# Kernel optimization log

Hardware: AMD Instinct MI355X
Metric: run time of the kernel (lower is better)

## Reference

```python
import jax, jax.numpy as jnp
import numpy as np

IOU_TH = 0.5      # iou_threshold
SCORE_TH = 0.5    # confidence_threshold (passed as score_threshold to tf NMS)
MAX_DET = 512     # max_detections


def setup_inputs() -> dict:
    key = jax.random.key(0)
    k1, k2, k3 = jax.random.split(key, 3)
    B, N, C = 8, 2048, 80
    # tf.image.non_max_suppression interprets box columns as corners
    # (y1, x1, y2, x2); generate valid corner boxes in [0, 1].
    mins = jax.random.uniform(k1, (B, N, 2), dtype=jnp.float32)
    sizes = jax.random.uniform(k2, (B, N, 2), dtype=jnp.float32) * 0.2 + 0.01
    box_prediction = jnp.concatenate([mins, mins + sizes], axis=-1)  # [B,N,4]
    class_prediction = jax.random.normal(k3, (B, N, C), dtype=jnp.float32) * 2.0
    return {"box_prediction": box_prediction, "class_prediction": class_prediction}


def _nms_single(boxes, cls_pred, conf):
    """Greedy NMS for one image. boxes [N,4], cls_pred [N,C], conf [N].
    Matches tf.image.non_max_suppression semantics (corner-coordinate IoU,
    score threshold, greedy suppression in descending score order),
    then gathers boxes/cls/conf at the kept indices, padded to MAX_DET."""
    N = boxes.shape[0]
    order = jnp.argsort(-conf)                 # descending scores
    b = boxes[order]                            # [N,4]
    c = cls_pred[order]                         # [N,C]
    s = conf[order]                             # [N]

    bb = jax.lax.stop_gradient(b)               # IoU/indices are non-diff
    y1, x1, y2, x2 = bb[:, 0], bb[:, 1], bb[:, 2], bb[:, 3]
    area = (y2 - y1) * (x2 - x1)                # [N]
    ih = jnp.clip(jnp.minimum(y2[:, None], y2[None, :]) -
                  jnp.maximum(y1[:, None], y1[None, :]), 0.0)
    iw = jnp.clip(jnp.minimum(x2[:, None], x2[None, :]) -
                  jnp.maximum(x1[:, None], x1[None, :]), 0.0)
    inter = ih * iw                             # [N,N]
    union = area[:, None] + area[None, :] - inter
    iou = inter / jnp.maximum(union, 1e-9)      # [N,N]

    valid = s > SCORE_TH                        # score_threshold filter
    idxs = jnp.arange(N)

    def step(keep, xs):
        row, i = xs
        # if box i survives, suppress all later boxes overlapping > IOU_TH
        sup = (row > IOU_TH) & (idxs > i) & keep[i]
        return keep & ~sup, None

    keep, _ = jax.lax.scan(step, valid, (iou, idxs))

    # select kept boxes (already sorted by score) padded to MAX_DET
    masked = jnp.where(keep, s, -1.0)
    top_s, top_idx = jax.lax.top_k(jax.lax.stop_gradient(masked), MAX_DET)
    vm = top_s > SCORE_TH                       # validity of each output slot
    out_box = b[top_idx] * vm[:, None].astype(b.dtype)
    out_cls = c[top_idx] * vm[:, None].astype(c.dtype)
    out_conf = jnp.where(vm, s[top_idx], 0.0)
    return out_box, out_cls, out_conf


def reference(box_prediction, class_prediction):
    # from_logits=True branch of the layer
    class_confidence = jnp.max(jax.nn.sigmoid(class_prediction), axis=-1)  # [B,N]
    cls_prob = jax.nn.softmax(class_prediction, axis=-1)                   # [B,N,C]
    nms_box, nms_cls, nms_conf = jax.vmap(_nms_single)(
        box_prediction, cls_prob, class_confidence)
    return nms_box, nms_cls, nms_conf
```

## Files before the change

kernel.cpp:

```cpp
#include <hip/hip_runtime.h>
#include <stdint.h>

#define BB 8
#define NN 2048
#define NC 80
#define MAXDET 512
#define WPR 32


#define ORD_HALF 0xBF000000u

__global__ __launch_bounds__(64) void k_conf(const float* __restrict__ cls,
                                             uint64_t* __restrict__ keys) {
    int gid = blockIdx.x * 64 + threadIdx.x;
    const float4* p = (const float4*)(cls + (size_t)gid * NC);
    float m = -3.0e38f;
#pragma unroll
    for (int i = 0; i < NC / 4; ++i) {
        float4 v = p[i];
        m = fmaxf(m, fmaxf(fmaxf(v.x, v.y), fmaxf(v.z, v.w)));
    }
    float e  = expf(-m);
    float cf = 1.0f / (1.0f + e);
    uint32_t u = __float_as_uint(cf);
    u = (u & 0x80000000u) ? ~u : (u | 0x80000000u);
    int n = gid & (NN - 1);
    keys[gid] = ((uint64_t)u << 32) | (uint32_t)(NN - 1 - n);
}

#define RCHUNK 128
__global__ __launch_bounds__(512) void k_rank(const uint64_t* __restrict__ keys_in,
                                              uint64_t* __restrict__ keys_out,
                                              const float* __restrict__ boxes,
                                              float* __restrict__ sboxes) {
    __shared__ uint64_t sk[NN];
    __shared__ uint16_t part[4][RCHUNK];
    int b = blockIdx.y, t = threadIdx.x;
    const uint64_t* kin = keys_in + (size_t)b * NN;
#pragma unroll
    for (int j = 0; j < NN / 512; ++j)
        sk[t + j * 512] = kin[t + j * 512];
    __syncthreads();
    int sub = t >> 7;
    int el  = t & (RCHUNK - 1);
    int e   = blockIdx.x * RCHUNK + el;
    uint64_t mykey = sk[e];
    int base = sub * (NN / 4);
    int r = 0;
    for (int mm = 0; mm < NN / 4; ++mm)
        r += (sk[base + mm] > mykey) ? 1 : 0;
    part[sub][el] = (uint16_t)r;
    __syncthreads();
    if (t < RCHUNK) {
        int rank = part[0][t] + part[1][t] + part[2][t] + part[3][t];
        keys_out[(size_t)b * NN + rank] = mykey;
        int orig = (NN - 1) - (int)(mykey & 0xFFFFFFFFull);
        ((float4*)sboxes)[(size_t)b * NN + rank] =
            ((const float4*)boxes)[(size_t)b * NN + orig];
    }
}

__global__ void k_sup(const float* __restrict__ sboxes, uint64_t* __restrict__ sup,
                      uint64_t* __restrict__ diagw) {
#pragma clang fp contract(off)
    __shared__ float cy1[256], cx1[256], cy2[256], cx2[256], car[256];
    __shared__ float ry1[64], rx1[64], ry2[64], rx2[64], rar[64];
    int rt = blockIdx.x, ct = blockIdx.y, b = blockIdx.z;
    int t = threadIdx.x;
    int col0 = ct << 8, row0 = rt << 6;
    {
        float4 bx = ((const float4*)sboxes)[(size_t)b * NN + col0 + t];
        cy1[t] = bx.x; cx1[t] = bx.y; cy2[t] = bx.z; cx2[t] = bx.w;
        car[t] = (bx.z - bx.x) * (bx.w - bx.y);
        if (t < 64) {
            float4 rb = ((const float4*)sboxes)[(size_t)b * NN + row0 + t];
            ry1[t] = rb.x; rx1[t] = rb.y; ry2[t] = rb.z; rx2[t] = rb.w;
            rar[t] = (rb.z - rb.x) * (rb.w - rb.y);
        }
    }
    __syncthreads();
    int lr = t & 63, lg = t >> 6;
    int r = row0 + lr;
    int gw = (ct << 2) + lg;
    int cbase = gw << 6;
    uint64_t w = 0;
    if (cbase + 63 > r) {
        float y1 = ry1[lr], x1 = rx1[lr], y2 = ry2[lr], x2 = rx2[lr], ar = rar[lr];
        int lcb = lg << 6;
        for (int c = 0; c < 64; ++c) {
            int lc = lcb + c;
            float ih = fmaxf(fminf(y2, cy2[lc]) - fmaxf(y1, cy1[lc]), 0.0f);
            float iw = fmaxf(fminf(x2, cx2[lc]) - fmaxf(x1, cx1[lc]), 0.0f);
            float inter = ih * iw;
            float uni = (ar + car[lc]) - inter;
            float iou = inter / fmaxf(uni, 1e-9f);
            if ((iou > 0.5f) & ((cbase + c) > r)) w |= (1ull << c);
        }
    }
    sup[((size_t)b * NN + r) * WPR + gw] = w;
    if (gw == (r >> 6)) diagw[(size_t)b * NN + r] = w;
}

__global__ __launch_bounds__(64) void k_nms(const uint64_t* __restrict__ keys,
                                            const float* __restrict__ sboxes,
                                            const uint64_t* __restrict__ sup,
                                            const uint64_t* __restrict__ diagw,
                                            int* __restrict__ kidx,
                                            int* __restrict__ kcount,
                                            float* __restrict__ out_box,
                                            float* __restrict__ out_conf) {
    __shared__ uint64_t kmaskS[WPR];
    __shared__ int pfx[WPR];
    __shared__ int s_kc;
    int b = blockIdx.x, t = threadIdx.x;
    const uint64_t* supb = sup + (size_t)b * NN * WPR;
    const uint64_t* keyb = keys + (size_t)b * NN;
    const uint64_t* dgb  = diagw + (size_t)b * NN;
    if (t < WPR) kmaskS[t] = 0;

    uint64_t kb = 0;
#pragma unroll 8
    for (int i = 0; i < WPR; ++i) {
        uint32_t hi = (uint32_t)(keyb[(i << 6) + t] >> 32);
        uint64_t bal = __ballot(hi > ORD_HALF);
        if (t == i) kb = ~bal;
    }

    int l2 = t & 31, half = t >> 5;
    uint64_t rows[32], rowsN[32];
    uint64_t diag, diagN = 0;
    {
        const uint64_t* rowp = supb + (size_t)(half << 5) * WPR + l2;
#pragma unroll
        for (int j = 0; j < 32; ++j) rows[j] = rowp[(size_t)j * WPR];
        diag = dgb[t];
    }

    int cnt = 0;
    for (int g = 0; g < WPR; ++g) {
        if (g + 1 < WPR) {
            const uint64_t* rowp = supb + (size_t)(((g + 1) << 6) + (half << 5)) * WPR + l2;
#pragma unroll
            for (int j = 0; j < 32; ++j) rowsN[j] = rowp[(size_t)j * WPR];
            diagN = dgb[((g + 1) << 6) + t];
        }
        uint32_t dlo = (uint32_t)diag, dhi = (uint32_t)(diag >> 32);
        uint64_t rwv = __shfl(kb, g);
        uint32_t rw_lo = __builtin_amdgcn_readfirstlane((uint32_t)rwv);
        uint32_t rw_hi = __builtin_amdgcn_readfirstlane((uint32_t)(rwv >> 32));
        uint64_t todo = ~(((uint64_t)rw_hi << 32) | rw_lo);
        uint64_t gm = 0;
        while (todo) {
            int c = __builtin_ctzll(todo);
            gm |= (1ull << c);
            uint32_t rlo = __builtin_amdgcn_readlane(dlo, c);
            uint32_t rhi = __builtin_amdgcn_readlane(dhi, c);
            todo &= ~((((uint64_t)rhi << 32) | rlo) | (1ull << c));
        }
        uint32_t gmh = half ? (uint32_t)(gm >> 32) : (uint32_t)gm;
        uint64_t acc = 0;
#pragma unroll
        for (int j = 0; j < 32; ++j)
            acc |= (((gmh >> j) & 1u) ? rows[j] : 0ull);
        acc |= __shfl(acc, t ^ 32);
        if (t < 32) kb |= acc;
        if (t == 0) kmaskS[g] = gm;
        cnt += __popcll(gm);
#pragma unroll
        for (int j = 0; j < 32; ++j) rows[j] = rowsN[j];
        diag = diagN;
        if (cnt >= MAXDET) break;
    }
    __syncthreads();

    if (t == 0) {
        int s = 0;
        for (int w2 = 0; w2 < WPR; ++w2) { pfx[w2] = s; s += __popcll(kmaskS[w2]); }
        s_kc = (s < MAXDET) ? s : MAXDET;
        kcount[b] = s_kc;
    }
    __syncthreads();
    for (int i = t; i < NN; i += 64) {
        uint64_t m = kmaskS[i >> 6];
        if ((m >> (i & 63)) & 1ull) {
            int rank = pfx[i >> 6] + __popcll(m & ((1ull << (i & 63)) - 1ull));
            if (rank < MAXDET) {
                ((float4*)out_box)[(size_t)b * MAXDET + rank] =
                    ((const float4*)sboxes)[(size_t)b * NN + i];
                uint64_t kk = keyb[i];
                uint32_t u = (uint32_t)(kk >> 32);
                float cf = (u & 0x80000000u) ? __uint_as_float(u ^ 0x80000000u)
                                             : __uint_as_float(~u);
                out_conf[(size_t)b * MAXDET + rank] = cf;
                kidx[b * MAXDET + rank] = (NN - 1) - (int)(kk & 0xFFFFFFFFull);
            }
        }
    }
    for (int k = s_kc + t; k < MAXDET; k += 64) {
        ((float4*)out_box)[(size_t)b * MAXDET + k] = make_float4(0.f, 0.f, 0.f, 0.f);
        out_conf[(size_t)b * MAXDET + k] = 0.0f;
    }
}

__global__ void k_softmax(const float* __restrict__ cls, const int* __restrict__ kidx,
                          const int* __restrict__ kcount, float* __restrict__ out_cls) {
    int k = blockIdx.x, b = blockIdx.y, lane = threadIdx.x;
    float* dst = out_cls + ((size_t)b * MAXDET + k) * NC;
    if (k >= kcount[b]) {
        dst[lane] = 0.0f;
        if (lane < NC - 64) dst[64 + lane] = 0.0f;
        return;
    }
    int n = kidx[b * MAXDET + k];
    const float* src = cls + ((size_t)b * NN + n) * NC;
    float x0 = src[lane];
    float x1 = (lane < NC - 64) ? src[64 + lane] : -3.0e38f;
    float m = fmaxf(x0, x1);
    for (int o = 32; o > 0; o >>= 1) m = fmaxf(m, __shfl_xor(m, o));
    float e0 = expf(x0 - m);
    float e1 = (lane < NC - 64) ? expf(x1 - m) : 0.0f;
    float s = e0 + e1;
    for (int o = 32; o > 0; o >>= 1) s += __shfl_xor(s, o);
    dst[lane] = e0 / s;
    if (lane < NC - 64) dst[64 + lane] = e1 / s;
}

extern "C" void kernel_launch(void* const* d_in, const int* in_sizes, int n_in,
                              void* d_out, int out_size, void* d_ws, size_t ws_size,
                              hipStream_t stream) {
    const float* boxes = (const float*)d_in[0];
    const float* cls   = (const float*)d_in[1];
    float* out      = (float*)d_out;
    float* out_box  = out;
    float* out_cls  = out + BB * MAXDET * 4;
    float* out_conf = out + BB * MAXDET * (4 + NC);

    char* ws = (char*)d_ws;
    uint64_t* keysA  = (uint64_t*)(ws + 0);
    uint64_t* keysB  = (uint64_t*)(ws + 131072);
    float*    sboxes = (float*)(ws + 262144);
    int*      kidx   = (int*)(ws + 524288);
    int*      kcount = (int*)(ws + 540672);
    uint64_t* diagw  = (uint64_t*)(ws + 540800);
    uint64_t* sup    = (uint64_t*)(ws + 671872);

    k_conf<<<(BB * NN) / 64, 64, 0, stream>>>(cls, keysA);
    k_rank<<<dim3(NN / RCHUNK, BB), 512, 0, stream>>>(keysA, keysB, boxes, sboxes);
    k_sup<<<dim3(NN / 64, NN / 256, BB), 256, 0, stream>>>(sboxes, sup, diagw);
    k_nms<<<BB, 64, 0, stream>>>(keysB, sboxes, sup, diagw, kidx, kcount, out_box, out_conf);
    k_softmax<<<dim3(MAXDET, BB), 64, 0, stream>>>(cls, kidx, kcount, out_cls);
}
```

Before: 86.94 us.

## Stage suppression row blocks through double-buffered LDS with coalesced loads in NMS

The greedy NMS kernel now copies each 64-row block of the suppression matrix into a double-buffered LDS tile using coalesced 16-byte loads. The next block is prefetched into registers while the current one is processed. The diagonal word is read from LDS, so the separate diagw array and its writes in k_sup are removed. This replaces strided per-lane global row loads with contiguous ones, at the cost of LDS traffic and a block barrier per iteration in a single-wave block.

```diff
diff --git a/kernel.cpp b/kernel.cpp
--- a/kernel.cpp
+++ b/kernel.cpp
@@ -60,8 +60,7 @@
     }
 }
 
-__global__ void k_sup(const float* __restrict__ sboxes, uint64_t* __restrict__ sup,
-                      uint64_t* __restrict__ diagw) {
+__global__ void k_sup(const float* __restrict__ sboxes, uint64_t* __restrict__ sup) {
 #pragma clang fp contract(off)
     __shared__ float cy1[256], cx1[256], cy2[256], cx2[256], car[256];
     __shared__ float ry1[64], rx1[64], ry2[64], rx2[64], rar[64];
@@ -98,24 +97,22 @@
         }
     }
     sup[((size_t)b * NN + r) * WPR + gw] = w;
-    if (gw == (r >> 6)) diagw[(size_t)b * NN + r] = w;
 }
 
 __global__ __launch_bounds__(64) void k_nms(const uint64_t* __restrict__ keys,
                                             const float* __restrict__ sboxes,
                                             const uint64_t* __restrict__ sup,
-                                            const uint64_t* __restrict__ diagw,
                                             int* __restrict__ kidx,
                                             int* __restrict__ kcount,
                                             float* __restrict__ out_box,
                                             float* __restrict__ out_conf) {
+    __shared__ uint64_t buf[2][64 * WPR];
     __shared__ uint64_t kmaskS[WPR];
     __shared__ int pfx[WPR];
     __shared__ int s_kc;
     int b = blockIdx.x, t = threadIdx.x;
     const uint64_t* supb = sup + (size_t)b * NN * WPR;
     const uint64_t* keyb = keys + (size_t)b * NN;
-    const uint64_t* dgb  = diagw + (size_t)b * NN;
     if (t < WPR) kmaskS[t] = 0;
 
     uint64_t kb = 0;
@@ -126,24 +123,25 @@
         if (t == i) kb = ~bal;
     }
 
+    {
+        const ulonglong2* src = (const ulonglong2*)supb;
+        ulonglong2* dst = (ulonglong2*)buf[0];
+#pragma unroll
+        for (int k2 = 0; k2 < 16; ++k2) dst[t + 64 * k2] = src[t + 64 * k2];
+    }
+    __syncthreads();
+
     int l2 = t & 31, half = t >> 5;
-    uint64_t rows[32], rowsN[32];
-    uint64_t diag, diagN = 0;
-    {
-        const uint64_t* rowp = supb + (size_t)(half << 5) * WPR + l2;
-#pragma unroll
-        for (int j = 0; j < 32; ++j) rows[j] = rowp[(size_t)j * WPR];
-        diag = dgb[t];
-    }
-
     int cnt = 0;
+    ulonglong2 stg[16];
     for (int g = 0; g < WPR; ++g) {
+        const uint64_t* cur = buf[g & 1];
         if (g + 1 < WPR) {
-            const uint64_t* rowp = supb + (size_t)(((g + 1) << 6) + (half << 5)) * WPR + l2;
-#pragma unroll
-            for (int j = 0; j < 32; ++j) rowsN[j] = rowp[(size_t)j * WPR];
-            diagN = dgb[((g + 1) << 6) + t];
-        }
+            const ulonglong2* src = (const ulonglong2*)(supb + (size_t)(g + 1) * 64 * WPR);
+#pragma unroll
+            for (int k2 = 0; k2 < 16; ++k2) stg[k2] = src[t + 64 * k2];
+        }
+        uint64_t diag = cur[t * WPR + g];
         uint32_t dlo = (uint32_t)diag, dhi = (uint32_t)(diag >> 32);
         uint64_t rwv = __shfl(kb, g);
         uint32_t rw_lo = __builtin_amdgcn_readfirstlane((uint32_t)rwv);
@@ -158,17 +156,23 @@
             todo &= ~((((uint64_t)rhi << 32) | rlo) | (1ull << c));
         }
         uint32_t gmh = half ? (uint32_t)(gm >> 32) : (uint32_t)gm;
+        const uint64_t* rowp = cur + ((half << 5) * WPR + l2);
         uint64_t acc = 0;
 #pragma unroll
-        for (int j = 0; j < 32; ++j)
-            acc |= (((gmh >> j) & 1u) ? rows[j] : 0ull);
+        for (int j = 0; j < 32; ++j) {
+            uint64_t row = rowp[(size_t)j * WPR];
+            acc |= (((gmh >> j) & 1u) ? row : 0ull);
+        }
         acc |= __shfl(acc, t ^ 32);
         if (t < 32) kb |= acc;
         if (t == 0) kmaskS[g] = gm;
         cnt += __popcll(gm);
-#pragma unroll
-        for (int j = 0; j < 32; ++j) rows[j] = rowsN[j];
-        diag = diagN;
+        if (g + 1 < WPR) {
+            ulonglong2* dst = (ulonglong2*)buf[(g + 1) & 1];
+#pragma unroll
+            for (int k2 = 0; k2 < 16; ++k2) dst[t + 64 * k2] = stg[k2];
+        }
+        __syncthreads();
         if (cnt >= MAXDET) break;
     }
     __syncthreads();
@@ -241,12 +245,11 @@
     float*    sboxes = (float*)(ws + 262144);
     int*      kidx   = (int*)(ws + 524288);
     int*      kcount = (int*)(ws + 540672);
-    uint64_t* diagw  = (uint64_t*)(ws + 540800);
-    uint64_t* sup    = (uint64_t*)(ws + 671872);
+    uint64_t* sup    = (uint64_t*)(ws + 540800);
 
     k_conf<<<(BB * NN) / 64, 64, 0, stream>>>(cls, keysA);
     k_rank<<<dim3(NN / RCHUNK, BB), 512, 0, stream>>>(keysA, keysB, boxes, sboxes);
-    k_sup<<<dim3(NN / 64, NN / 256, BB), 256, 0, stream>>>(sboxes, sup, diagw);
-    k_nms<<<BB, 64, 0, stream>>>(keysB, sboxes, sup, diagw, kidx, kcount, out_box, out_conf);
+    k_sup<<<dim3(NN / 64, NN / 256, BB), 256, 0, stream>>>(sboxes, sup);
+    k_nms<<<BB, 64, 0, stream>>>(keysB, sboxes, sup, kidx, kcount, out_box, out_conf);
     k_softmax<<<dim3(MAXDET, BB), 64, 0, stream>>>(cls, kidx, kcount, out_cls);
 }
```

Result: slower. 97.14 us (+11.7%).
